# Kernel optimization log

Measured on AMD Instinct MI355X. Metric: run time of the kernel, lower is better.

Reference implementation:

```python
import math
import jax, jax.numpy as jnp
import numpy as np

WIN = 8
NUM_HEADS = 8

def _rel_pos_index(win):
    coords = np.stack(np.meshgrid(np.arange(win), np.arange(win), indexing='ij'))
    cf = coords.reshape(2, -1)
    rel = cf[:, :, None] - cf[:, None, :]
    rel = rel.transpose(1, 2, 0).copy()
    rel[:, :, 0] += win - 1
    rel[:, :, 1] += win - 1
    rel[:, :, 0] *= 2 * win - 1
    return rel.sum(-1)  # [N, N]

def _shift_mask(H, W, win, Ho, Wo):
    m = np.zeros((H, W))
    h_slices = (slice(0, -win), slice(-win, -Ho), slice(-Ho, None)) if Ho > 0 else (slice(0, None),)
    w_slices = (slice(0, -win), slice(-win, -Wo), slice(-Wo, None)) if Wo > 0 else (slice(0, None),)
    cnt = 0
    for hs in h_slices:
        for ws in w_slices:
            m[hs, ws] = cnt
            cnt += 1
    mw = m.reshape(H // win, win, W // win, win).transpose(0, 2, 1, 3).reshape(-1, win * win)
    d = mw[:, None, :] - mw[:, :, None]
    return np.where(d != 0, -100.0, 0.0).astype(np.float32)  # [nW, N, N]

def _ln(x, g, b, eps=1e-5):
    mu = jnp.mean(x, axis=-1, keepdims=True)
    var = jnp.mean((x - mu) ** 2, axis=-1, keepdims=True)
    return (x - mu) / jnp.sqrt(var + eps) * g + b

def _win_part(x, win):
    B, H, W, C = x.shape
    x = x.reshape(B, H // win, win, W // win, win, C).transpose(0, 1, 3, 2, 4, 5)
    return x.reshape(-1, win * win, C)

def _win_rev(w, win, H, W):
    C = w.shape[-1]
    B = w.shape[0] // ((H // win) * (W // win))
    x = w.reshape(B, H // win, W // win, win, win, C).transpose(0, 1, 3, 2, 4, 5)
    return x.reshape(B, H, W, C)

def setup_inputs() -> dict:
    key = jax.random.key(0)
    ks = jax.random.split(key, 10)
    B, L, C, hid = 4, 32768, 256, 1024
    s = 0.02
    return {
        'x': jax.random.normal(ks[0], (B, L, C), jnp.float32),
        'norm1_g': jnp.ones((C,), jnp.float32),
        'norm1_b': jnp.zeros((C,), jnp.float32),
        'wq': jax.random.normal(ks[1], (C, C), jnp.float32) * s,
        'bq': jnp.zeros((C,), jnp.float32),
        'wv': jax.random.normal(ks[2], (C, C), jnp.float32) * s,
        'bv': jnp.zeros((C,), jnp.float32),
        'rpb': jax.random.normal(ks[3], (225, NUM_HEADS), jnp.float32) * s,
        'wproj': jax.random.normal(ks[4], (C, C), jnp.float32) * s,
        'bproj': jnp.zeros((C,), jnp.float32),
        'norm2_g': jnp.ones((C,), jnp.float32),
        'norm2_b': jnp.zeros((C,), jnp.float32),
        'w1': jax.random.normal(ks[5], (C, hid), jnp.float32) * s,
        'b1': jnp.zeros((hid,), jnp.float32),
        'dw_k': jax.random.normal(ks[6], (hid, 1, 3, 3), jnp.float32) * s,
        'dw_b': jnp.zeros((hid,), jnp.float32),
        'w2': jax.random.normal(ks[7], (hid, C), jnp.float32) * s,
        'b2': jnp.zeros((C,), jnp.float32),
        'H_offset': 3,
        'W_offset': 5,
    }

def reference(x, norm1_g, norm1_b, wq, bq, wv, bv, rpb, wproj, bproj,
              norm2_g, norm2_b, w1, b1, dw_k, dw_b, w2, b2, H_offset, W_offset):
    B, L, C = x.shape
    H = int(round(math.sqrt(L * 2)))
    W = int(round(math.sqrt(L // 2)))
    win, h = WIN, NUM_HEADS
    hd = C // h
    N = win * win
    nW = (H // win) * (W // win)
    scale = hd ** -0.5

    shortcut = x
    xn = _ln(x, norm1_g, norm1_b)
    q = xn @ wq + bq
    v = xn @ wv + bv
    q = q.reshape(B, H, W, C)
    v = v.reshape(B, H, W, C)
    k = q  # module uses k = q (shared)

    q = jnp.roll(q, (-H_offset, -W_offset), axis=(1, 2))
    k = jnp.roll(k, (-H_offset, -W_offset), axis=(1, 2))
    v = jnp.roll(v, (-H_offset, -W_offset), axis=(1, 2))

    qw = _win_part(q, win).reshape(-1, N, h, hd).transpose(0, 2, 1, 3)
    kw = _win_part(k, win).reshape(-1, N, h, hd).transpose(0, 2, 1, 3)
    vw = _win_part(v, win).reshape(-1, N, h, hd).transpose(0, 2, 1, 3)

    attn = jnp.einsum('bhnd,bhmd->bhnm', qw * scale, kw)
    bias = rpb[jnp.asarray(_rel_pos_index(win).reshape(-1))].reshape(N, N, h).transpose(2, 0, 1)
    attn = attn + bias[None]
    mask = jnp.asarray(_shift_mask(H, W, win, int(H_offset), int(W_offset)))
    attn = (attn.reshape(B, nW, h, N, N) + mask[None, :, None]).reshape(-1, h, N, N)
    attn = jax.nn.softmax(attn, axis=-1)

    y = jnp.einsum('bhnm,bhmd->bhnd', attn, vw).transpose(0, 2, 1, 3).reshape(-1, N, C)
    y = y @ wproj + bproj
    y = _win_rev(y.reshape(-1, win, win, C), win, H, W)
    y = jnp.roll(y, (H_offset, W_offset), axis=(1, 2)).reshape(B, L, C)

    x = shortcut + y

    # LeFF
    xn2 = _ln(x, norm2_g, norm2_b)
    t = jax.nn.gelu(xn2 @ w1 + b1, approximate=False)  # [B, L, hid]
    t = t.reshape(B, H, W, -1).transpose(0, 3, 1, 2)   # NCHW
    t = jax.lax.conv_general_dilated(t, dw_k, (1, 1), 'SAME',
                                     feature_group_count=t.shape[1],
                                     dimension_numbers=('NCHW', 'OIHW', 'NCHW'))
    t = jax.nn.gelu(t + dw_b[None, :, None, None], approximate=False)
    t = t.transpose(0, 2, 3, 1).reshape(B, L, -1)
    t = t @ w2 + b2
    return x + t
```

## Files before the change

kernel.cpp:

```cpp
#include <hip/hip_runtime.h>
#include <stdint.h>
#include <math.h>

#define H_IMG 256
#define W_IMG 128
#define LTOK  32768
#define BATCH 4
#define CDIM  256
#define HIDDIM 1024
#define NHEAD 8
#define HD    32
#define MROWS 131072

typedef __attribute__((ext_vector_type(8))) short short8;
typedef __attribute__((ext_vector_type(4))) float f32x4;

__device__ __forceinline__ float bf2f(unsigned u) {
  union { unsigned u; float f; } c; c.u = u << 16; return c.f;
}
__device__ __forceinline__ unsigned short f2bf(float f) {
  union { float f; unsigned u; } c; c.f = f;
  unsigned r = c.u + 0x7fffu + ((c.u >> 16) & 1u);
  return (unsigned short)(r >> 16);
}
__device__ __forceinline__ float gelu_f(float x) {
  return 0.5f * x * (1.0f + erff(x * 0.70710678118654752f));
}
__device__ __forceinline__ void gload_lds16(const void* g, void* l) {
  __builtin_amdgcn_global_load_lds(
      (const __attribute__((address_space(1))) unsigned int*)g,
      (__attribute__((address_space(3))) unsigned int*)l, 16, 0, 0);
}

__global__ __launch_bounds__(256) void wconv_kernel(
    const float* __restrict__ w, unsigned short* __restrict__ wt, int K, int N) {
  __shared__ float t[32][33];
  const int k0 = blockIdx.x * 32, n0 = blockIdx.y * 32;
  const int tx = threadIdx.x & 31, ty = threadIdx.x >> 5;
#pragma unroll
  for (int i = 0; i < 4; ++i)
    t[ty + 8 * i][tx] = w[(size_t)(k0 + ty + 8 * i) * N + n0 + tx];
  __syncthreads();
#pragma unroll
  for (int i = 0; i < 4; ++i)
    wt[(size_t)(n0 + ty + 8 * i) * K + k0 + tx] = f2bf(t[tx][ty + 8 * i]);
}

__global__ __launch_bounds__(256) void ln_kernel(
    const float* __restrict__ x, const float* __restrict__ g,
    const float* __restrict__ b, unsigned short* __restrict__ out) {
  const int wave = threadIdx.x >> 6;
  const int lane = threadIdx.x & 63;
  const size_t row = (size_t)blockIdx.x * 4 + wave;
  float4 f = ((const float4*)(x + row * CDIM))[lane];
  float s  = f.x + f.y + f.z + f.w;
  float sq = f.x*f.x + f.y*f.y + f.z*f.z + f.w*f.w;
#pragma unroll
  for (int o = 32; o > 0; o >>= 1) { s += __shfl_down(s, o); sq += __shfl_down(sq, o); }
  s = __shfl(s, 0); sq = __shfl(sq, 0);
  const float mu = s * (1.0f / CDIM);
  const float var = sq * (1.0f / CDIM) - mu * mu;
  const float rstd = rsqrtf(var + 1e-5f);
  float4 gg = ((const float4*)g)[lane];
  float4 bb = ((const float4*)b)[lane];
  unsigned short o4[4];
  o4[0] = f2bf((f.x - mu) * rstd * gg.x + bb.x);
  o4[1] = f2bf((f.y - mu) * rstd * gg.y + bb.y);
  o4[2] = f2bf((f.z - mu) * rstd * gg.z + bb.z);
  o4[3] = f2bf((f.w - mu) * rstd * gg.w + bb.w);
  *(uint2*)(out + row * CDIM + lane * 4) = *(uint2*)o4;
}

template<int EPI, int PERM>
__global__ __launch_bounds__(256) void mgemm(
    const unsigned short* __restrict__ A, const unsigned short* __restrict__ Bt,
    const float* __restrict__ bias, float bscale, const float* __restrict__ res,
    void* __restrict__ outp, int K, int ldc,
    const int* __restrict__ pHo, const int* __restrict__ pWo) {
  __shared__ unsigned short As[2][128][32];
  __shared__ unsigned short Bs[2][128][32];
  const int tid = threadIdx.x;
  const int w = tid >> 6, lane = tid & 63;
  const int m0 = blockIdx.x * 128, n0 = blockIdx.y * 128;
  const int wm = (w & 1) * 64, wn = (w >> 1) * 64;
  const int srow = lane >> 2;
  const int csrc = (lane & 3) ^ (srow & 3);
  f32x4 acc[4][4];
#pragma unroll
  for (int mi = 0; mi < 4; ++mi)
#pragma unroll
    for (int ni = 0; ni < 4; ++ni)
#pragma unroll
      for (int r = 0; r < 4; ++r) acc[mi][ni][r] = 0.0f;

  const int kg = lane >> 4, ml = lane & 15;
  const int nt = K >> 5;

  auto STAGE = [&](int kk, int buf) {
#pragma unroll
    for (int i = 0; i < 2; ++i) {
      const int rl = w * 32 + i * 16 + srow;
      gload_lds16(A + (size_t)(m0 + rl) * K + kk + csrc * 8, &As[buf][w * 32 + i * 16][0]);
      gload_lds16(Bt + (size_t)(n0 + rl) * K + kk + csrc * 8, &Bs[buf][w * 32 + i * 16][0]);
    }
  };

  STAGE(0, 0);
  for (int t = 0; t < nt; ++t) {
    const int cur = t & 1;
    if (t + 1 < nt) {
      STAGE((t + 1) << 5, cur ^ 1);
      asm volatile("s_waitcnt vmcnt(4)" ::: "memory");
    } else {
      asm volatile("s_waitcnt vmcnt(0)" ::: "memory");
    }
    __builtin_amdgcn_s_barrier();
    __builtin_amdgcn_sched_barrier(0);
    short8 af[4], bg[4];
#pragma unroll
    for (int mi = 0; mi < 4; ++mi) {
      const int r = wm + mi * 16 + ml;
      af[mi] = *(const short8*)&As[cur][r][(kg ^ (r & 3)) * 8];
    }
#pragma unroll
    for (int ni = 0; ni < 4; ++ni) {
      const int r = wn + ni * 16 + ml;
      bg[ni] = *(const short8*)&Bs[cur][r][(kg ^ (r & 3)) * 8];
    }
#pragma unroll
    for (int mi = 0; mi < 4; ++mi)
#pragma unroll
      for (int ni = 0; ni < 4; ++ni)
        acc[mi][ni] = __builtin_amdgcn_mfma_f32_16x16x32_bf16(af[mi], bg[ni], acc[mi][ni], 0, 0, 0);
    __builtin_amdgcn_sched_barrier(0);
    __builtin_amdgcn_s_barrier();
  }

  const int Ho = (PERM == 1 || PERM == 2 || PERM == 3) ? pHo[0] : 0;
  const int Wo = (PERM == 1 || PERM == 2 || PERM == 3) ? pWo[0] : 0;
  size_t ridx[4][4];
#pragma unroll
  for (int mi = 0; mi < 4; ++mi) {
#pragma unroll
    for (int r = 0; r < 4; ++r) {
      const int m = m0 + wm + mi * 16 + kg * 4 + r;
      if constexpr (PERM == 1 || PERM == 2) {
        const int bimg = m >> 15, l = m & 32767;
        const int hq = l >> 7, wq_ = l & 127;
        int hr = hq - Ho; if (hr < 0) hr += H_IMG;
        int wr = wq_ - Wo; if (wr < 0) wr += W_IMG;
        const int win = (hr >> 3) * 16 + (wr >> 3);
        const int t64 = (hr & 7) * 8 + (wr & 7);
        ridx[mi][r] = (size_t)(bimg * 512 + win) * 16384 +
                      (PERM == 1 ? t64 * 32 : t64);
      } else if constexpr (PERM == 3) {
        const int bimg = m >> 15, win = (m >> 6) & 511, t64 = m & 63;
        int h = (win >> 4) * 8 + (t64 >> 3) + Ho; if (h >= H_IMG) h -= H_IMG;
        int ww_ = (win & 15) * 8 + (t64 & 7) + Wo; if (ww_ >= W_IMG) ww_ -= W_IMG;
        ridx[mi][r] = ((size_t)(bimg << 15) + h * W_IMG + ww_) * ldc;
      } else {
        ridx[mi][r] = (size_t)m * ldc;
      }
    }
  }
#pragma unroll
  for (int ni = 0; ni < 4; ++ni) {
    const int n = n0 + wn + ni * 16 + ml;
    const float bn = bias[n] * bscale;
    size_t noff;
    if constexpr (PERM == 1)      noff = (size_t)(n >> 5) * 2048 + (n & 31);
    else if constexpr (PERM == 2) noff = (size_t)(n >> 5) * 2048 + (n & 31) * 64;
    else                          noff = (size_t)n;
#pragma unroll
    for (int mi = 0; mi < 4; ++mi) {
#pragma unroll
      for (int r = 0; r < 4; ++r) {
        const size_t idx = ridx[mi][r] + noff;
        float val = acc[mi][ni][r] + bn;
        if (EPI == 1) {
          ((float*)outp)[idx] = val + res[idx];
        } else if (EPI == 2) {
          ((unsigned short*)outp)[idx] = f2bf(gelu_f(val));
        } else {
          ((unsigned short*)outp)[idx] = f2bf(val);
        }
      }
    }
  }
}

__global__ __launch_bounds__(256, 3) void attn_kernel(
    const unsigned short* __restrict__ q, const unsigned short* __restrict__ v,
    const float* __restrict__ rpb, const int* __restrict__ pHo,
    const int* __restrict__ pWo, unsigned short* __restrict__ yout) {
  __shared__ unsigned short Pb[4][4096];
  __shared__ float bias_w[4][228];
  __shared__ int reg_s[64];
  const int tid = threadIdx.x;
  const int w = tid >> 6, lane = tid & 63;
  const int g = lane >> 4, c = lane & 15;
  const int wb = blockIdx.x;
  const int b = wb >> 9, wloc = wb & 511;
  const int wh = wloc >> 4, ww = wloc & 15;
  const int Ho = pHo[0], Wo = pWo[0];
  const bool edge = (wh == (H_IMG / 8 - 1)) || (ww == (W_IMG / 8 - 1));
  if (w == 0) {
    const int dy = lane >> 3, dx = lane & 7;
    const int hr = wh * 8 + dy, wr = ww * 8 + dx;
    const int rh = (hr < H_IMG - 8) ? 0 : ((hr < H_IMG - Ho) ? 1 : 2);
    const int rw = (wr < W_IMG - 8) ? 0 : ((wr < W_IMG - Wo) ? 1 : 2);
    reg_s[lane] = rh * 3 + rw;
  }
  __syncthreads();

  const float scale = 0.17677669529663687f;
  const int dxk = c & 7, dyk0 = c >> 3;
  const int base_l = 112 - dyk0 * 15 - dxk;
  const size_t hbase0 = (size_t)(b * 512 + wloc) * 8;

  for (int p2 = 0; p2 < 2; ++p2) {
    const int hh = w + 4 * p2;
    const unsigned short* qh = q + (hbase0 + hh) * 2048;
    const unsigned short* vh = v + (hbase0 + hh) * 2048;
#pragma unroll
    for (int i = 0; i < 4; ++i) {
      const int idx = lane + 64 * i;
      if (idx < 225) bias_w[w][idx] = rpb[idx * 8 + hh];
    }
    short8 q4[4];
#pragma unroll
    for (int mi = 0; mi < 4; ++mi)
      q4[mi] = *(const short8*)(qh + (16 * mi + c) * 32 + g * 8);
    short8 vf[2][2];
#pragma unroll
    for (int s2 = 0; s2 < 2; ++s2)
#pragma unroll
      for (int n2 = 0; n2 < 2; ++n2)
        vf[s2][n2] = *(const short8*)(vh + (16 * n2 + c) * 64 + 32 * s2 + 8 * g);
    f32x4 acc[4][4];
#pragma unroll
    for (int mi = 0; mi < 4; ++mi)
#pragma unroll
      for (int nj = 0; nj < 4; ++nj)
#pragma unroll
        for (int r = 0; r < 4; ++r) acc[mi][nj][r] = 0.0f;
#pragma unroll
    for (int mi = 0; mi < 4; ++mi)
#pragma unroll
      for (int nj = 0; nj < 4; ++nj)
        acc[mi][nj] = __builtin_amdgcn_mfma_f32_16x16x32_bf16(q4[mi], q4[nj], acc[mi][nj], 0, 0, 0);
    int regk[4];
    if (edge) {
#pragma unroll
      for (int nj = 0; nj < 4; ++nj) regk[nj] = reg_s[16 * nj + c];
    }
    unsigned short* Pp = &Pb[w][0];
    float ivr[4][4];
#pragma unroll
    for (int mi = 0; mi < 4; ++mi) {
#pragma unroll
      for (int r = 0; r < 4; ++r) {
        const int qq = 16 * mi + 4 * g + r;
        const int rb = (qq >> 3) * 15 + (qq & 7) + base_l;
        float sv[4];
#pragma unroll
        for (int nj = 0; nj < 4; ++nj)
          sv[nj] = acc[mi][nj][r] * scale + bias_w[w][rb - 30 * nj];
        if (edge) {
          const int regq = reg_s[qq];
#pragma unroll
          for (int nj = 0; nj < 4; ++nj)
            if (regq != regk[nj]) sv[nj] -= 100.0f;
        }
        float e0 = __expf(sv[0]), e1 = __expf(sv[1]);
        float e2 = __expf(sv[2]), e3 = __expf(sv[3]);
        float sm = e0 + e1 + e2 + e3;
        sm += __shfl_xor(sm, 1);
        sm += __shfl_xor(sm, 2);
        sm += __shfl_xor(sm, 4);
        sm += __shfl_xor(sm, 8);
        ivr[mi][r] = __builtin_amdgcn_rcpf(sm);
        const int rowoff = qq * 64, sw = qq & 7;
        Pp[rowoff + ((dyk0 ^ sw) * 8)       + dxk] = f2bf(e0);
        Pp[rowoff + (((2 + dyk0) ^ sw) * 8) + dxk] = f2bf(e1);
        Pp[rowoff + (((4 + dyk0) ^ sw) * 8) + dxk] = f2bf(e2);
        Pp[rowoff + (((6 + dyk0) ^ sw) * 8) + dxk] = f2bf(e3);
      }
    }
    f32x4 oacc[4][2];
#pragma unroll
    for (int mi = 0; mi < 4; ++mi)
#pragma unroll
      for (int n2 = 0; n2 < 2; ++n2)
#pragma unroll
        for (int r = 0; r < 4; ++r) oacc[mi][n2][r] = 0.0f;
#pragma unroll
    for (int s2 = 0; s2 < 2; ++s2) {
      short8 pa[4];
#pragma unroll
      for (int mi = 0; mi < 4; ++mi) {
        const int qq2 = 16 * mi + c;
        pa[mi] = *(const short8*)&Pp[qq2 * 64 + (((4 * s2 + g) ^ (qq2 & 7)) * 8)];
      }
#pragma unroll
      for (int mi = 0; mi < 4; ++mi)
#pragma unroll
        for (int n2 = 0; n2 < 2; ++n2)
          oacc[mi][n2] = __builtin_amdgcn_mfma_f32_16x16x32_bf16(pa[mi], vf[s2][n2], oacc[mi][n2], 0, 0, 0);
    }
    unsigned short* Ost = Pp;
#pragma unroll
    for (int mi = 0; mi < 4; ++mi)
#pragma unroll
      for (int n2 = 0; n2 < 2; ++n2)
#pragma unroll
        for (int r = 0; r < 4; ++r)
          Ost[(16 * mi + 4 * g + r) * 40 + 16 * n2 + c] = f2bf(oacc[mi][n2][r] * ivr[mi][r]);
    uint4* op = (uint4*)(yout + ((size_t)(b * 512 + wloc) * 64 + lane) * 256 + hh * 32);
#pragma unroll
    for (int u = 0; u < 4; ++u)
      op[u] = *(const uint4*)&Ost[lane * 40 + u * 8];
  }
}

__global__ __launch_bounds__(256) void dwconv_kernel(
    const unsigned short* __restrict__ t1b, const float* __restrict__ k9,
    const float* __restrict__ bias, unsigned short* __restrict__ t2b,
    int hr0, int band_rows) {
  const int c = blockIdx.y * 128 + (threadIdx.x & 31) * 4;
  const int tok = blockIdx.x * 8 + (threadIdx.x >> 5);
  const int h = hr0 + (tok >> 7), wcol = tok & 127;
  float wreg[4][9];
#pragma unroll
  for (int j = 0; j < 4; ++j)
#pragma unroll
    for (int tp = 0; tp < 9; ++tp) wreg[j][tp] = k9[(c + j) * 9 + tp];
  const float4 bv = *(const float4*)(bias + c);
  float a0 = 0, a1 = 0, a2 = 0, a3 = 0;
#pragma unroll
  for (int ky = 0; ky < 3; ++ky) {
    const int hy = h + ky - 1;
    if ((unsigned)hy >= (unsigned)H_IMG) continue;
    const int brow = (tok >> 7) + ky;
#pragma unroll
    for (int kx = 0; kx < 3; ++kx) {
      const int wx = wcol + kx - 1;
      if ((unsigned)wx >= (unsigned)W_IMG) continue;
      const ushort4 tv = *(const ushort4*)(
          t1b + ((size_t)(brow * 128 + wx)) * HIDDIM + c);
      const int tp = ky * 3 + kx;
      a0 += bf2f(tv.x) * wreg[0][tp];
      a1 += bf2f(tv.y) * wreg[1][tp];
      a2 += bf2f(tv.z) * wreg[2][tp];
      a3 += bf2f(tv.w) * wreg[3][tp];
    }
  }
  a0 = gelu_f(a0 + bv.x); a1 = gelu_f(a1 + bv.y);
  a2 = gelu_f(a2 + bv.z); a3 = gelu_f(a3 + bv.w);
  unsigned short o[4] = { f2bf(a0), f2bf(a1), f2bf(a2), f2bf(a3) };
  *(uint2*)(t2b + (size_t)tok * HIDDIM + c) = *(uint2*)o;
}

extern "C" void kernel_launch(void* const* d_in, const int* in_sizes, int n_in,
                              void* d_out, int out_size, void* d_ws, size_t ws_size,
                              hipStream_t stream) {
  (void)in_sizes; (void)n_in; (void)out_size; (void)ws_size;
  const float* x     = (const float*)d_in[0];
  const float* n1g   = (const float*)d_in[1];
  const float* n1b   = (const float*)d_in[2];
  const float* wq    = (const float*)d_in[3];
  const float* bq    = (const float*)d_in[4];
  const float* wv    = (const float*)d_in[5];
  const float* bv    = (const float*)d_in[6];
  const float* rpb   = (const float*)d_in[7];
  const float* wproj = (const float*)d_in[8];
  const float* bproj = (const float*)d_in[9];
  const float* n2g   = (const float*)d_in[10];
  const float* n2b   = (const float*)d_in[11];
  const float* w1    = (const float*)d_in[12];
  const float* b1    = (const float*)d_in[13];
  const float* dwk   = (const float*)d_in[14];
  const float* dwb   = (const float*)d_in[15];
  const float* w2    = (const float*)d_in[16];
  const float* b2    = (const float*)d_in[17];
  const int*   pHo   = (const int*)d_in[18];
  const int*   pWo   = (const int*)d_in[19];
  float* out = (float*)d_out;

  char* wsb = (char*)d_ws;
  unsigned short* r0     = (unsigned short*)wsb;
  unsigned short* wqt    = (unsigned short*)(wsb + 67108864ull);
  unsigned short* wvt    = (unsigned short*)(wsb + 67108864ull + 131072ull);
  unsigned short* wprojt = (unsigned short*)(wsb + 67108864ull + 262144ull);
  unsigned short* w1t    = (unsigned short*)(wsb + 67108864ull + 393216ull);
  unsigned short* w2t    = (unsigned short*)(wsb + 67108864ull + 917504ull);
  unsigned short* t1b    = (unsigned short*)(wsb + 68550656ull);
  unsigned short* t2b    = (unsigned short*)(wsb + 68550656ull + 25690112ull);
  unsigned short* vb     = (unsigned short*)d_out;
  unsigned short* qb     = (unsigned short*)((char*)d_out + 67108864ull);

  wconv_kernel<<<dim3(8, 8),  256, 0, stream>>>(wq,    wqt,    CDIM, CDIM);
  wconv_kernel<<<dim3(8, 8),  256, 0, stream>>>(wv,    wvt,    CDIM, CDIM);
  wconv_kernel<<<dim3(8, 8),  256, 0, stream>>>(wproj, wprojt, CDIM, CDIM);
  wconv_kernel<<<dim3(8, 32), 256, 0, stream>>>(w1,    w1t,    CDIM, HIDDIM);
  wconv_kernel<<<dim3(32, 8), 256, 0, stream>>>(w2,    w2t,    HIDDIM, CDIM);

  ln_kernel<<<32768, 256, 0, stream>>>(x, n1g, n1b, r0);
  mgemm<0, 1><<<dim3(1024, 2), 256, 0, stream>>>(r0, wqt, bq, 1.0f, nullptr, qb, CDIM, CDIM, pHo, pWo);
  mgemm<0, 2><<<dim3(1024, 2), 256, 0, stream>>>(r0, wvt, bv, 1.0f, nullptr, vb, CDIM, CDIM, pHo, pWo);
  attn_kernel<<<dim3(2048), 256, 0, stream>>>(qb, vb, rpb, pHo, pWo, r0);
  mgemm<1, 3><<<dim3(1024, 2), 256, 0, stream>>>(r0, wprojt, bproj, 1.0f, x, out, CDIM, CDIM, pHo, pWo);
  ln_kernel<<<32768, 256, 0, stream>>>(out, n2g, n2b, r0);
  for (int bi = 0; bi < BATCH; ++bi) {
    for (int hr0 = 0; hr0 < H_IMG; ) {
      const int br = (H_IMG - hr0 >= 96) ? 96 : (H_IMG - hr0);
      const int r_start = (hr0 > 0) ? hr0 - 1 : 0;
      const int r_end = (hr0 + br <= H_IMG - 1) ? hr0 + br : H_IMG - 1;
      const int nrows = r_end - r_start + 1;
      const unsigned short* Aff1 = r0 + ((size_t)bi * LTOK + (size_t)r_start * W_IMG) * CDIM;
      unsigned short* t1dst = t1b + (size_t)(r_start - hr0 + 1) * W_IMG * HIDDIM;
      mgemm<2, 0><<<dim3(nrows, 8), 256, 0, stream>>>(
          Aff1, w1t, b1, 1.0f, nullptr, t1dst, CDIM, HIDDIM, pHo, pWo);
      dwconv_kernel<<<dim3(br * 16, 8), 256, 0, stream>>>(t1b, dwk, dwb, t2b, hr0, br);
      const size_t btok = (size_t)bi * LTOK + (size_t)hr0 * W_IMG;
      mgemm<1, 0><<<dim3(br, 2), 256, 0, stream>>>(
          t2b, w2t, b2, 1.0f, out + btok * CDIM, out + btok * CDIM, HIDDIM, CDIM, pHo, pWo);
      hr0 += br;
    }
  }
}
```

Before: 1.656 ms.

## Fuse Q/V projection GEMMs, move window-reverse scatter into attention, widen dwconv

The separate Q and V projection GEMMs become one launch over a 4-wide N grid, and each block picks its output buffer, bias and permuted layout from its N offset. The inverse window permutation and roll move from the proj GEMM epilogue into the attention kernel's output store, so the proj GEMM does plain row-major stores with the residual. The depthwise conv now handles 8 channels per thread with 16-byte loads instead of 4. The intent is fewer launches, cheaper GEMM epilogue addressing, and wider memory accesses, at the cost of scattered token-order writes from attention and more registers in dwconv.

```diff
diff --git a/kernel.cpp b/kernel.cpp
--- a/kernel.cpp
+++ b/kernel.cpp
@@ -22,6 +22,12 @@
   union { float f; unsigned u; } c; c.f = f;
   unsigned r = c.u + 0x7fffu + ((c.u >> 16) & 1u);
   return (unsigned short)(r >> 16);
+}
+__device__ __forceinline__ void unpack8(uint4 t, float* dst) {
+  dst[0] = bf2f(t.x & 0xffffu); dst[1] = bf2f(t.x >> 16);
+  dst[2] = bf2f(t.y & 0xffffu); dst[3] = bf2f(t.y >> 16);
+  dst[4] = bf2f(t.z & 0xffffu); dst[5] = bf2f(t.z >> 16);
+  dst[6] = bf2f(t.w & 0xffffu); dst[7] = bf2f(t.w >> 16);
 }
 __device__ __forceinline__ float gelu_f(float x) {
   return 0.5f * x * (1.0f + erff(x * 0.70710678118654752f));
@@ -74,9 +80,9 @@
 template<int EPI, int PERM>
 __global__ __launch_bounds__(256) void mgemm(
     const unsigned short* __restrict__ A, const unsigned short* __restrict__ Bt,
-    const float* __restrict__ bias, float bscale, const float* __restrict__ res,
-    void* __restrict__ outp, int K, int ldc,
-    const int* __restrict__ pHo, const int* __restrict__ pWo) {
+    const float* __restrict__ bias, const float* __restrict__ bias2,
+    const float* __restrict__ res, void* __restrict__ outp, void* __restrict__ outp2,
+    int K, int ldc, const int* __restrict__ pHo, const int* __restrict__ pWo) {
   __shared__ unsigned short As[2][128][32];
   __shared__ unsigned short Bs[2][128][32];
   const int tid = threadIdx.x;
@@ -136,53 +142,55 @@
     __builtin_amdgcn_s_barrier();
   }
 
-  const int Ho = (PERM == 1 || PERM == 2 || PERM == 3) ? pHo[0] : 0;
-  const int Wo = (PERM == 1 || PERM == 2 || PERM == 3) ? pWo[0] : 0;
-  size_t ridx[4][4];
-#pragma unroll
-  for (int mi = 0; mi < 4; ++mi) {
-#pragma unroll
-    for (int r = 0; r < 4; ++r) {
-      const int m = m0 + wm + mi * 16 + kg * 4 + r;
-      if constexpr (PERM == 1 || PERM == 2) {
+  if constexpr (PERM == 4) {
+    const int Ho = pHo[0], Wo = pWo[0];
+    const bool vhalf = (n0 >= 256);
+    size_t rbase[4][4];
+#pragma unroll
+    for (int mi = 0; mi < 4; ++mi) {
+#pragma unroll
+      for (int r = 0; r < 4; ++r) {
+        const int m = m0 + wm + mi * 16 + kg * 4 + r;
         const int bimg = m >> 15, l = m & 32767;
-        const int hq = l >> 7, wq_ = l & 127;
-        int hr = hq - Ho; if (hr < 0) hr += H_IMG;
-        int wr = wq_ - Wo; if (wr < 0) wr += W_IMG;
+        int hr = (l >> 7) - Ho; if (hr < 0) hr += H_IMG;
+        int wr = (l & 127) - Wo; if (wr < 0) wr += W_IMG;
         const int win = (hr >> 3) * 16 + (wr >> 3);
         const int t64 = (hr & 7) * 8 + (wr & 7);
-        ridx[mi][r] = (size_t)(bimg * 512 + win) * 16384 +
-                      (PERM == 1 ? t64 * 32 : t64);
-      } else if constexpr (PERM == 3) {
-        const int bimg = m >> 15, win = (m >> 6) & 511, t64 = m & 63;
-        int h = (win >> 4) * 8 + (t64 >> 3) + Ho; if (h >= H_IMG) h -= H_IMG;
-        int ww_ = (win & 15) * 8 + (t64 & 7) + Wo; if (ww_ >= W_IMG) ww_ -= W_IMG;
-        ridx[mi][r] = ((size_t)(bimg << 15) + h * W_IMG + ww_) * ldc;
-      } else {
-        ridx[mi][r] = (size_t)m * ldc;
+        rbase[mi][r] = (size_t)(bimg * 512 + win) * 16384 + (vhalf ? t64 : t64 * 32);
       }
     }
-  }
-#pragma unroll
-  for (int ni = 0; ni < 4; ++ni) {
-    const int n = n0 + wn + ni * 16 + ml;
-    const float bn = bias[n] * bscale;
-    size_t noff;
-    if constexpr (PERM == 1)      noff = (size_t)(n >> 5) * 2048 + (n & 31);
-    else if constexpr (PERM == 2) noff = (size_t)(n >> 5) * 2048 + (n & 31) * 64;
-    else                          noff = (size_t)n;
-#pragma unroll
-    for (int mi = 0; mi < 4; ++mi) {
-#pragma unroll
-      for (int r = 0; r < 4; ++r) {
-        const size_t idx = ridx[mi][r] + noff;
-        float val = acc[mi][ni][r] + bn;
-        if (EPI == 1) {
-          ((float*)outp)[idx] = val + res[idx];
-        } else if (EPI == 2) {
-          ((unsigned short*)outp)[idx] = f2bf(gelu_f(val));
-        } else {
-          ((unsigned short*)outp)[idx] = f2bf(val);
+    unsigned short* dst = (unsigned short*)(vhalf ? outp2 : outp);
+    const float* bp = vhalf ? bias2 : bias;
+#pragma unroll
+    for (int ni = 0; ni < 4; ++ni) {
+      const int nn = n0 + wn + ni * 16 + ml - (vhalf ? 256 : 0);
+      const float bn = bp[nn];
+      const size_t noff = (size_t)(nn >> 5) * 2048 + (vhalf ? (nn & 31) * 64 : (nn & 31));
+#pragma unroll
+      for (int mi = 0; mi < 4; ++mi)
+#pragma unroll
+        for (int r = 0; r < 4; ++r)
+          dst[rbase[mi][r] + noff] = f2bf(acc[mi][ni][r] + bn);
+    }
+  } else {
+#pragma unroll
+    for (int ni = 0; ni < 4; ++ni) {
+      const int n = n0 + wn + ni * 16 + ml;
+      const float bn = bias[n];
+#pragma unroll
+      for (int mi = 0; mi < 4; ++mi) {
+#pragma unroll
+        for (int r = 0; r < 4; ++r) {
+          const int m = m0 + wm + mi * 16 + kg * 4 + r;
+          const size_t idx = (size_t)m * ldc + n;
+          float val = acc[mi][ni][r] + bn;
+          if (EPI == 1) {
+            ((float*)outp)[idx] = val + res[idx];
+          } else if (EPI == 2) {
+            ((unsigned short*)outp)[idx] = f2bf(gelu_f(val));
+          } else {
+            ((unsigned short*)outp)[idx] = f2bf(val);
+          }
         }
       }
     }
@@ -217,6 +225,10 @@
   const int dxk = c & 7, dyk0 = c >> 3;
   const int base_l = 112 - dyk0 * 15 - dxk;
   const size_t hbase0 = (size_t)(b * 512 + wloc) * 8;
+  const int dy2 = lane >> 3, dx2 = lane & 7;
+  int h2 = wh * 8 + dy2 + Ho; if (h2 >= H_IMG) h2 -= H_IMG;
+  int w2_ = ww * 8 + dx2 + Wo; if (w2_ >= W_IMG) w2_ -= W_IMG;
+  const size_t otok = (size_t)b * LTOK + (size_t)h2 * W_IMG + w2_;
 
   for (int p2 = 0; p2 < 2; ++p2) {
     const int hh = w + 4 * p2;
@@ -316,7 +328,7 @@
 #pragma unroll
         for (int r = 0; r < 4; ++r)
           Ost[(16 * mi + 4 * g + r) * 40 + 16 * n2 + c] = f2bf(oacc[mi][n2][r] * ivr[mi][r]);
-    uint4* op = (uint4*)(yout + ((size_t)(b * 512 + wloc) * 64 + lane) * 256 + hh * 32);
+    uint4* op = (uint4*)(yout + otok * CDIM + hh * 32);
 #pragma unroll
     for (int u = 0; u < 4; ++u)
       op[u] = *(const uint4*)&Ost[lane * 40 + u * 8];
@@ -327,16 +339,18 @@
     const unsigned short* __restrict__ t1b, const float* __restrict__ k9,
     const float* __restrict__ bias, unsigned short* __restrict__ t2b,
     int hr0, int band_rows) {
-  const int c = blockIdx.y * 128 + (threadIdx.x & 31) * 4;
+  const int c = blockIdx.y * 256 + (threadIdx.x & 31) * 8;
   const int tok = blockIdx.x * 8 + (threadIdx.x >> 5);
   const int h = hr0 + (tok >> 7), wcol = tok & 127;
-  float wreg[4][9];
-#pragma unroll
-  for (int j = 0; j < 4; ++j)
+  float wreg[8][9];
+#pragma unroll
+  for (int j = 0; j < 8; ++j)
 #pragma unroll
     for (int tp = 0; tp < 9; ++tp) wreg[j][tp] = k9[(c + j) * 9 + tp];
-  const float4 bv = *(const float4*)(bias + c);
-  float a0 = 0, a1 = 0, a2 = 0, a3 = 0;
+  float bb[8];
+#pragma unroll
+  for (int j = 0; j < 8; ++j) bb[j] = bias[c + j];
+  float a[8] = {};
 #pragma unroll
   for (int ky = 0; ky < 3; ++ky) {
     const int hy = h + ky - 1;
@@ -346,19 +360,19 @@
     for (int kx = 0; kx < 3; ++kx) {
       const int wx = wcol + kx - 1;
       if ((unsigned)wx >= (unsigned)W_IMG) continue;
-      const ushort4 tv = *(const ushort4*)(
+      const uint4 tv = *(const uint4*)(
           t1b + ((size_t)(brow * 128 + wx)) * HIDDIM + c);
+      float f8[8];
+      unpack8(tv, f8);
       const int tp = ky * 3 + kx;
-      a0 += bf2f(tv.x) * wreg[0][tp];
-      a1 += bf2f(tv.y) * wreg[1][tp];
-      a2 += bf2f(tv.z) * wreg[2][tp];
-      a3 += bf2f(tv.w) * wreg[3][tp];
-    }
-  }
-  a0 = gelu_f(a0 + bv.x); a1 = gelu_f(a1 + bv.y);
-  a2 = gelu_f(a2 + bv.z); a3 = gelu_f(a3 + bv.w);
-  unsigned short o[4] = { f2bf(a0), f2bf(a1), f2bf(a2), f2bf(a3) };
-  *(uint2*)(t2b + (size_t)tok * HIDDIM + c) = *(uint2*)o;
+#pragma unroll
+      for (int j = 0; j < 8; ++j) a[j] += f8[j] * wreg[j][tp];
+    }
+  }
+  unsigned short o[8];
+#pragma unroll
+  for (int j = 0; j < 8; ++j) o[j] = f2bf(gelu_f(a[j] + bb[j]));
+  *(uint4*)(t2b + (size_t)tok * HIDDIM + c) = *(uint4*)o;
 }
 
 extern "C" void kernel_launch(void* const* d_in, const int* in_sizes, int n_in,
@@ -406,10 +420,11 @@
   wconv_kernel<<<dim3(32, 8), 256, 0, stream>>>(w2,    w2t,    HIDDIM, CDIM);
 
   ln_kernel<<<32768, 256, 0, stream>>>(x, n1g, n1b, r0);
-  mgemm<0, 1><<<dim3(1024, 2), 256, 0, stream>>>(r0, wqt, bq, 1.0f, nullptr, qb, CDIM, CDIM, pHo, pWo);
-  mgemm<0, 2><<<dim3(1024, 2), 256, 0, stream>>>(r0, wvt, bv, 1.0f, nullptr, vb, CDIM, CDIM, pHo, pWo);
+  mgemm<0, 4><<<dim3(1024, 4), 256, 0, stream>>>(
+      r0, wqt, bq, bv, nullptr, qb, vb, CDIM, CDIM, pHo, pWo);
   attn_kernel<<<dim3(2048), 256, 0, stream>>>(qb, vb, rpb, pHo, pWo, r0);
-  mgemm<1, 3><<<dim3(1024, 2), 256, 0, stream>>>(r0, wprojt, bproj, 1.0f, x, out, CDIM, CDIM, pHo, pWo);
+  mgemm<1, 0><<<dim3(1024, 2), 256, 0, stream>>>(
+      r0, wprojt, bproj, nullptr, x, out, nullptr, CDIM, CDIM, pHo, pWo);
   ln_kernel<<<32768, 256, 0, stream>>>(out, n2g, n2b, r0);
   for (int bi = 0; bi < BATCH; ++bi) {
     for (int hr0 = 0; hr0 < H_IMG; ) {
@@ -420,11 +435,12 @@
       const unsigned short* Aff1 = r0 + ((size_t)bi * LTOK + (size_t)r_start * W_IMG) * CDIM;
       unsigned short* t1dst = t1b + (size_t)(r_start - hr0 + 1) * W_IMG * HIDDIM;
       mgemm<2, 0><<<dim3(nrows, 8), 256, 0, stream>>>(
-          Aff1, w1t, b1, 1.0f, nullptr, t1dst, CDIM, HIDDIM, pHo, pWo);
-      dwconv_kernel<<<dim3(br * 16, 8), 256, 0, stream>>>(t1b, dwk, dwb, t2b, hr0, br);
+          Aff1, w1t, b1, nullptr, nullptr, t1dst, nullptr, CDIM, HIDDIM, pHo, pWo);
+      dwconv_kernel<<<dim3(br * 16, 4), 256, 0, stream>>>(t1b, dwk, dwb, t2b, hr0, br);
       const size_t btok = (size_t)bi * LTOK + (size_t)hr0 * W_IMG;
       mgemm<1, 0><<<dim3(br, 2), 256, 0, stream>>>(
-          t2b, w2t, b2, 1.0f, out + btok * CDIM, out + btok * CDIM, HIDDIM, CDIM, pHo, pWo);
+          t2b, w2t, b2, nullptr, out + btok * CDIM, out + btok * CDIM, nullptr,
+          HIDDIM, CDIM, pHo, pWo);
       hr0 += br;
     }
   }
```

New measurement: 1.644 ms. About the same (-0.7%).
